# Kernel optimization log

Hardware: AMD Instinct MI355X
Metric: run time of the kernel (lower is better)

The kernel has to match this reference:

```python
import jax, jax.numpy as jnp
import numpy as np

B, S, P, D = 128, 64, 32, 256   # batch, seq_len, pad_size, input_size
E, H, L, A, O = 256, 128, 2, 1, 2  # embed, hidden, n_layers, att_dim, output
INITRANGE = 0.1


def setup_inputs() -> dict:
    key = jax.random.key(0)
    ks = jax.random.split(key, 12)
    u = lambda k, shape: jax.random.uniform(k, shape, jnp.float32, -INITRANGE, INITRANGE)
    return {
        "inputs": jax.random.normal(ks[0], (B, S, P, D), jnp.float32),
        "conv_w": u(ks[1], (D,)),          # Conv1d(1,1,kernel=D) weight (output length is 1)
        "conv_b": u(ks[2], (1,)),
        "embed_w": u(ks[3], (E, D)),       # Linear(D,E,bias=False)
        "gru_Wih": u(ks[4], (L, 2, 3 * H, E)),  # [layer, direction, 3H, in] (E == 2H)
        "gru_Whh": u(ks[5], (L, 2, 3 * H, H)),
        "gru_bih": u(ks[6], (L, 2, 3 * H)),
        "gru_bhh": u(ks[7], (L, 2, 3 * H)),
        "att_w1": u(ks[8], (A, 2 * H)),    # Linear(2H, att_dim, bias=False)
        "lin_w": u(ks[9], (O, 2 * H)),
        "lin_b": u(ks[10], (O,)),
        "batch_size": B,
    }


def _gru_layer(x, Wih, Whh, bih, bhh, reverse):
    # x: [B,S,Din]; torch GRU cell semantics.
    xg = jnp.einsum('bsd,gd->sbg', x, Wih) + bih  # precompute input gates [S,B,3H]
    h0 = jnp.zeros((x.shape[0], Whh.shape[1]), x.dtype)

    def step(h, xg_t):
        gh = h @ Whh.T + bhh
        xr, xz, xn = jnp.split(xg_t, 3, axis=-1)
        hr, hz, hn = jnp.split(gh, 3, axis=-1)
        r = jax.nn.sigmoid(xr + hr)
        z = jax.nn.sigmoid(xz + hz)
        n = jnp.tanh(xn + r * hn)
        h_new = (1.0 - z) * n + z * h
        return h_new, h_new

    _, hs = jax.lax.scan(step, h0, xg, reverse=reverse)  # [S,B,H], time-aligned
    return jnp.swapaxes(hs, 0, 1)  # [B,S,H]


def _forward(inputs, conv_w, conv_b, embed_w, gru_Wih, gru_Whh, gru_bih, gru_bhh,
             att_w1, lin_w, lin_b, batch_size):
    # convolutional_layer: conv output length is 1 -> per-event scalar dot product,
    # then bmm gives a weighted sum of events within each visit.
    s = jnp.einsum('bspk,k->bsp', inputs, conv_w) + conv_b[0]      # [B,S,P]
    conv_all = jnp.einsum('bsp,bspk->bsk', s, inputs)               # [B,S,D]
    # embedding_layer: Linear(D,E) + Hardtanh
    x = jnp.clip(conv_all @ embed_w.T, -1.0, 1.0)                   # [B,S,E]
    # bidirectional multi-layer GRU, h0 = zeros (dropout_p = 0 -> identity)
    for l in range(L):
        f = _gru_layer(x, gru_Wih[l, 0], gru_Whh[l, 0], gru_bih[l, 0], gru_bhh[l, 0], False)
        b = _gru_layer(x, gru_Wih[l, 1], gru_Whh[l, 1], gru_bih[l, 1], gru_bhh[l, 1], True)
        x = jnp.concatenate([f, b], axis=-1)                        # [B,S,2H]
    states = x
    # add_attention: per-step Linear(2H, att_dim) + softmax over att_dim (nn.Softmax on [B,A])
    alpha = jax.nn.softmax(jnp.einsum('bsh,ah->bsa', states, att_w1), axis=-1)
    alpha = jnp.swapaxes(alpha, 1, 2)                               # [B,A,S]
    context = jnp.einsum('bas,bsh->bah', alpha, states).reshape(batch_size, -1)  # [B, A*2H]
    out = jax.nn.softmax(context @ lin_w.T + lin_b, axis=-1)        # [B,O]
    return out, states, context, alpha


def reference(inputs, conv_w, conv_b, embed_w, gru_Wih, gru_Whh, gru_bih, gru_bhh,
              att_w1, lin_w, lin_b, batch_size):
    return _forward(inputs, conv_w, conv_b, embed_w, gru_Wih, gru_Whh, gru_bih,
                    gru_bhh, att_w1, lin_w, lin_b, batch_size)
```

## Files before the change

### kernel.cpp

```cpp
#include <hip/hip_runtime.h>


using u16 = unsigned short;
using u32 = unsigned int;

typedef __bf16    bf16x8 __attribute__((ext_vector_type(8)));
typedef _Float16  f16x8  __attribute__((ext_vector_type(8)));
typedef float     f32x4  __attribute__((ext_vector_type(4)));

__device__ __forceinline__ float bf2f(u16 u) {
  union { u32 i; float f; } v; v.i = ((u32)u) << 16; return v.f;
}
__device__ __forceinline__ u16 f2bf(float f) {
  union { float f; u32 i; } v; v.f = f;
  u32 i = v.i;
  u32 r = (i + 0x7FFFu + ((i >> 16) & 1u)) >> 16;
  return (u16)r;
}
__device__ __forceinline__ float sigm(float x) { return 1.f / (1.f + __expf(-x)); }
__device__ __forceinline__ float tanh_f(float x) { return 1.f - 2.f / (1.f + __expf(2.f * x)); }

__global__ __launch_bounds__(256) void k_conv(
    const float* __restrict__ inp, const float* __restrict__ cw,
    const float* __restrict__ cb, u16* __restrict__ chi, u16* __restrict__ clo,
    const float* __restrict__ embw, const float* __restrict__ Wih,
    u16* __restrict__ embHi, u16* __restrict__ embLo, u16* __restrict__ wihB) {
  __shared__ float tile[32 * 256];
  __shared__ float cwf[256];
  __shared__ float s_p[32];
  const int bs  = blockIdx.x;
  const int tid = threadIdx.x;
  const float* src = inp + (size_t)bs * 8192;
#pragma unroll
  for (int i = 0; i < 8; i++) {
    int idx = i * 1024 + tid * 4;
    *(float4*)&tile[idx] = *(const float4*)&src[idx];
  }
  cwf[tid] = cw[tid];
  if (bs < 1536) {
    const int i = bs * 256 + tid;
    if (i < 65536) {
      float v = embw[i];
      u16 h = f2bf(v);
      embHi[i] = h;
      embLo[i] = f2bf(v - bf2f(h));
    }
    wihB[i] = f2bf(Wih[i]);
  }
  __syncthreads();
  const int wv = tid >> 6, ln = tid & 63;
  const float cbf = cb[0];
  for (int pp = 0; pp < 8; pp++) {
    int p = wv * 8 + pp;
    float part = 0.f;
#pragma unroll
    for (int q = 0; q < 4; q++) {
      int k = ln + q * 64;
      part += tile[p * 256 + k] * cwf[k];
    }
    for (int off = 32; off; off >>= 1) part += __shfl_xor(part, off, 64);
    if (ln == 0) s_p[p] = part + cbf;
  }
  __syncthreads();
  float acc = 0.f;
  const int k = tid;
#pragma unroll
  for (int p = 0; p < 32; p++) acc += s_p[p] * tile[p * 256 + k];
  u16 hi = f2bf(acc);
  float lo = acc - bf2f(hi);
  chi[(size_t)bs * 256 + k] = hi;
  clo[(size_t)bs * 256 + k] = f2bf(lo);
}

template <bool HAS_ALO, bool HAS_WLO, bool HAS_BIAS, bool CLIP, bool OUT_BF16>
__global__ __launch_bounds__(256) void k_gemm(
    const u16* __restrict__ A, const u16* __restrict__ Alo,
    const u16* __restrict__ W, const u16* __restrict__ Wlo,
    const float* __restrict__ bias,
    void* __restrict__ Cout, int M, int N, int K) {
  const int LDT = 56;
  __shared__ u16 As[64 * 56];
  __shared__ u16 La[64 * 56];
  __shared__ u16 Ws[64 * 56];
  __shared__ u16 Lw[64 * 56];
  const int tid = threadIdx.x;
  const int m0 = blockIdx.x * 64, n0 = blockIdx.y * 64;
  const int wv = tid >> 6, ln = tid & 63;
  const int lm = ln & 15, lk = (ln >> 4) * 8;
  const int srow = tid >> 2, sgrp = tid & 3;

  const size_t aRow = (size_t)(m0 + srow) * K + sgrp * 8;
  const size_t wRow = (size_t)(n0 + srow) * K + sgrp * 8;

  f32x4 acc[4];
#pragma unroll
  for (int nt = 0; nt < 4; nt++) acc[nt] = (f32x4){0.f, 0.f, 0.f, 0.f};

  uint4 rA = *(const uint4*)&A[aRow];
  uint4 rW = *(const uint4*)&W[wRow];
  uint4 rLa, rLw;
  if (HAS_ALO) rLa = *(const uint4*)&Alo[aRow];
  if (HAS_WLO) rLw = *(const uint4*)&Wlo[wRow];

  const int nIter = K >> 5;
  for (int it = 0; it < nIter; it++) {
    __syncthreads();
    *(uint4*)&As[srow * LDT + sgrp * 8] = rA;
    *(uint4*)&Ws[srow * LDT + sgrp * 8] = rW;
    if (HAS_ALO) *(uint4*)&La[srow * LDT + sgrp * 8] = rLa;
    if (HAS_WLO) *(uint4*)&Lw[srow * LDT + sgrp * 8] = rLw;
    if (it + 1 < nIter) {
      const int kc = (it + 1) * 32;
      rA = *(const uint4*)&A[aRow + kc];
      rW = *(const uint4*)&W[wRow + kc];
      if (HAS_ALO) rLa = *(const uint4*)&Alo[aRow + kc];
      if (HAS_WLO) rLw = *(const uint4*)&Wlo[wRow + kc];
    }
    __syncthreads();

    bf16x8 af = *(const bf16x8*)&As[(wv * 16 + lm) * LDT + lk];
    bf16x8 bfr[4];
#pragma unroll
    for (int nt = 0; nt < 4; nt++)
      bfr[nt] = *(const bf16x8*)&Ws[(nt * 16 + lm) * LDT + lk];
#pragma unroll
    for (int nt = 0; nt < 4; nt++)
      acc[nt] = __builtin_amdgcn_mfma_f32_16x16x32_bf16(af, bfr[nt], acc[nt], 0, 0, 0);
    if (HAS_ALO) {
      bf16x8 lf = *(const bf16x8*)&La[(wv * 16 + lm) * LDT + lk];
#pragma unroll
      for (int nt = 0; nt < 4; nt++)
        acc[nt] = __builtin_amdgcn_mfma_f32_16x16x32_bf16(lf, bfr[nt], acc[nt], 0, 0, 0);
    }
    if (HAS_WLO) {
#pragma unroll
      for (int nt = 0; nt < 4; nt++) {
        bf16x8 wl = *(const bf16x8*)&Lw[(nt * 16 + lm) * LDT + lk];
        acc[nt] = __builtin_amdgcn_mfma_f32_16x16x32_bf16(af, wl, acc[nt], 0, 0, 0);
      }
    }
  }

  const int rbase = m0 + wv * 16 + (ln >> 4) * 4;
#pragma unroll
  for (int nt = 0; nt < 4; nt++) {
    const int col = n0 + nt * 16 + lm;
    const float bv = HAS_BIAS ? bias[col] : 0.f;
#pragma unroll
    for (int r = 0; r < 4; r++) {
      float v = acc[nt][r] + bv;
      if (CLIP) v = fminf(fmaxf(v, -1.f), 1.f);
      const int row = rbase + r;
      if (OUT_BF16)
        ((u16*)Cout)[(size_t)row * N + col] = f2bf(v);
      else
        ((float*)Cout)[(size_t)row * N + col] = v;
    }
  }
}

__global__ __launch_bounds__(512, 2) void k_gru(
    const u16* __restrict__ xsrc,
    const u16* __restrict__ wihL,
    const float* __restrict__ bihL,
    const float* __restrict__ WhhL,
    const float* __restrict__ bhhL,
    float* __restrict__ xg,
    u16* __restrict__ st_bf,
    float* __restrict__ st_f,
    float* __restrict__ ctx) {
  __shared__ __attribute__((aligned(16))) u16 xt[64 * 264];
  __shared__ __attribute__((aligned(16))) _Float16 hbHi[2][128];
  __shared__ __attribute__((aligned(16))) _Float16 hbLo[2][128];

  const int b   = blockIdx.x >> 1;
  const int dir = blockIdx.x & 1;
  const int tid = threadIdx.x;
  const int w   = tid >> 6, l = tid & 63;
  const int lm  = l & 15;
  const int kw  = (l >> 4) * 8;
  const int d   = w * 16 + lm;

  f16x8 whi[3][4], wlo[3][4];
#pragma unroll
  for (int tt = 0; tt < 3; tt++) {
#pragma unroll
    for (int kt = 0; kt < 4; kt++) {
      const int row = (tt * 8 + w) * 16 + lm;
      const float* p = WhhL + ((size_t)(dir * 384 + row)) * 128 + kt * 32 + kw;
      union { f16x8 v; _Float16 s[8]; } Wh, Wl;
#pragma unroll
      for (int j = 0; j < 8; j++) {
        float v = p[j];
        _Float16 h = (_Float16)v;
        Wh.s[j] = h;
        Wl.s[j] = (_Float16)(v - (float)h);
      }
      whi[tt][kt] = Wh.v;
      wlo[tt][kt] = Wl.v;
    }
  }

  const u16*   wihD = wihL + (size_t)dir * 98304;
  const float* bihD = bihL + dir * 384;
  float*       xgc  = xg + (size_t)(b * 2 + dir) * 24576;
  {
    const u16* xrow = xsrc + (size_t)(b * 64) * 256;
#pragma unroll
    for (int it = 0; it < 4; it++) {
      const int idx = it * 512 + tid;
      const int r = idx >> 5, c8 = (idx & 31) * 8;
      *(uint4*)&xt[r * 264 + c8] = *(const uint4*)&xrow[r * 256 + c8];
    }
    __syncthreads();
#pragma unroll
    for (int tt = 0; tt < 3; tt++) {
      const int nt = tt * 8 + w;
      bf16x8 bfr[8];
#pragma unroll
      for (int kk = 0; kk < 8; kk++)
        bfr[kk] = *(const bf16x8*)&wihD[(size_t)(nt * 16 + lm) * 256 + kk * 32 + kw];
      const float bv = bihD[nt * 16 + lm];
      const int col = nt * 16 + lm;
#pragma unroll
      for (int mt = 0; mt < 4; mt++) {
        f32x4 a4 = (f32x4){0.f, 0.f, 0.f, 0.f};
#pragma unroll
        for (int kk = 0; kk < 8; kk++) {
          bf16x8 af = *(const bf16x8*)&xt[(mt * 16 + lm) * 264 + kk * 32 + kw];
          a4 = __builtin_amdgcn_mfma_f32_16x16x32_bf16(af, bfr[kk], a4, 0, 0, 0);
        }
        const int trow = mt * 16 + (l >> 4) * 4;
#pragma unroll
        for (int r = 0; r < 4; r++)
          xgc[(size_t)(trow + r) * 384 + col] = a4[r] + bv;
      }
    }
  }
  float bhr = 0.f, bhz = 0.f, bhn = 0.f;
  if (l < 16) {
    bhr = bhhL[dir * 384 + d];
    bhz = bhhL[dir * 384 + 128 + d];
    bhn = bhhL[dir * 384 + 256 + d];
  }
  if (tid < 128) { hbHi[0][tid] = (_Float16)0.f; hbLo[0][tid] = (_Float16)0.f; }
  __syncthreads();

  const float* xbase = xgc + d;
  float xr = 0.f, xz = 0.f, xn = 0.f;
  if (l < 16) {
    const int t0 = dir ? 63 : 0;
    xr = xbase[t0 * 384];
    xz = xbase[t0 * 384 + 128];
    xn = xbase[t0 * 384 + 256];
  }
  float hold = 0.f, csum = 0.f;

  int cur = 0;
  for (int ti = 0; ti < 64; ti++) {
    const int t = dir ? (63 - ti) : ti;
    float nxr = 0.f, nxz = 0.f, nxn = 0.f;
    if (l < 16 && ti < 63) {
      const int tn = dir ? (62 - ti) : (ti + 1);
      nxr = xbase[tn * 384];
      nxz = xbase[tn * 384 + 128];
      nxn = xbase[tn * 384 + 256];
    }
    const _Float16* hsrc = (l & 1) ? hbLo[cur] : hbHi[cur];
    f16x8 af[4];
#pragma unroll
    for (int kt = 0; kt < 4; kt++)
      af[kt] = *(const f16x8*)&hsrc[kt * 32 + kw];

    f32x4 aH[3], aL[3];
#pragma unroll
    for (int tt = 0; tt < 3; tt++) {
      aH[tt] = (f32x4){0.f, 0.f, 0.f, 0.f};
      aL[tt] = (f32x4){0.f, 0.f, 0.f, 0.f};
    }
#pragma unroll
    for (int kt = 0; kt < 4; kt++) {
#pragma unroll
      for (int tt = 0; tt < 3; tt++) {
        aH[tt] = __builtin_amdgcn_mfma_f32_16x16x32_f16(af[kt], whi[tt][kt], aH[tt], 0, 0, 0);
        aL[tt] = __builtin_amdgcn_mfma_f32_16x16x32_f16(af[kt], wlo[tt][kt], aL[tt], 0, 0, 0);
      }
    }
    const int nxt = cur ^ 1;
    if (l < 16) {
      const float ghr = aH[0][0] + aH[0][1] + aL[0][0] + aL[0][1];
      const float ghz = aH[1][0] + aH[1][1] + aL[1][0] + aL[1][1];
      const float ghn = aH[2][0] + aH[2][1] + aL[2][0] + aL[2][1];
      const float rg = sigm(xr + bhr + ghr);
      const float zg = sigm(xz + bhz + ghz);
      const float ng = tanh_f(xn + rg * (ghn + bhn));
      const float hn = (1.f - zg) * ng + zg * hold;
      hold = hn;
      csum += hn;
      const _Float16 hh = (_Float16)hn;
      hbHi[nxt][d] = hh;
      hbLo[nxt][d] = (_Float16)(hn - (float)hh);
      const size_t oi = (size_t)(b * 64 + t) * 256 + dir * 128 + d;
      if (st_bf) st_bf[oi] = f2bf(hn);
      if (st_f)  st_f[oi]  = hn;
    }
    asm volatile("s_waitcnt lgkmcnt(0)" ::: "memory");
    __builtin_amdgcn_s_barrier();
    cur = nxt;
    xr = nxr; xz = nxz; xn = nxn;
  }
  if (ctx != nullptr && l < 16)
    ctx[(size_t)b * 256 + dir * 128 + d] = csum;
}

__global__ __launch_bounds__(64) void k_final(
    const float* __restrict__ ctx, const float* __restrict__ lw,
    const float* __restrict__ lb, float* __restrict__ out,
    float* __restrict__ alpha) {
  const int b = blockIdx.x;
  const int l = threadIdx.x;
  float a0 = 0.f, a1 = 0.f;
#pragma unroll
  for (int q = 0; q < 4; q++) {
    const int k = q * 64 + l;
    const float c = ctx[b * 256 + k];
    a0 += c * lw[k];
    a1 += c * lw[256 + k];
  }
  for (int off = 32; off; off >>= 1) {
    a0 += __shfl_xor(a0, off, 64);
    a1 += __shfl_xor(a1, off, 64);
  }
  alpha[b * 64 + l] = 1.0f;
  if (l == 0) {
    a0 += lb[0];
    a1 += lb[1];
    const float m = fmaxf(a0, a1);
    const float e0 = __expf(a0 - m), e1 = __expf(a1 - m);
    const float s = e0 + e1;
    out[2 * b]     = e0 / s;
    out[2 * b + 1] = e1 / s;
  }
}

extern "C" void kernel_launch(void* const* d_in, const int* in_sizes, int n_in,
                              void* d_out, int out_size, void* d_ws, size_t ws_size,
                              hipStream_t stream) {
  const float* inp   = (const float*)d_in[0];
  const float* convw = (const float*)d_in[1];
  const float* convb = (const float*)d_in[2];
  const float* embw  = (const float*)d_in[3];
  const float* Wih   = (const float*)d_in[4];
  const float* Whh   = (const float*)d_in[5];
  const float* bih   = (const float*)d_in[6];
  const float* bhh   = (const float*)d_in[7];
  const float* lw    = (const float*)d_in[9];
  const float* lb    = (const float*)d_in[10];

  char* ws = (char*)d_ws;
  u16*   convHi = (u16*)(ws);
  u16*   convLo = (u16*)(ws + 4194304u);
  u16*   xbuf   = (u16*)(ws + 8388608u);
  u16*   embHi  = (u16*)(ws + 12582912u);
  u16*   embLo  = (u16*)(ws + 12713984u);
  u16*   wihB   = (u16*)(ws + 12845056u);
  float* xgbuf  = (float*)(ws + 13631488u);
  u16*   states0 = convHi;

  float* outp    = (float*)d_out;
  float* statesO = outp + 256;
  float* ctxO    = outp + 2097408;
  float* alphaO  = outp + 2130176;

  k_conv<<<8192, 256, 0, stream>>>(inp, convw, convb, convHi, convLo,
                                   embw, Wih, embHi, embLo, wihB);

  dim3 gE(128, 4);
  k_gemm<true, true, false, true, true><<<gE, 256, 0, stream>>>(
      convHi, convLo, embHi, embLo, nullptr, xbuf, 8192, 256, 256);

  k_gru<<<256, 512, 0, stream>>>(xbuf, wihB, bih, Whh, bhh, xgbuf,
                                 states0, nullptr, nullptr);

  k_gru<<<256, 512, 0, stream>>>(states0, wihB + 196608, bih + 768,
                                 Whh + 98304, bhh + 768, xgbuf,
                                 nullptr, statesO, ctxO);

  k_final<<<128, 64, 0, stream>>>(ctxO, lw, lb, outp, alphaO);
}
```

Before: 528.1 us.

## Fuse embedding GEMM into first GRU layer kernel

Measured after the change: 541.0 us. 1.02x slower.

```diff
diff --git a/kernel.cpp b/kernel.cpp
--- a/kernel.cpp
+++ b/kernel.cpp
@@ -72,95 +72,13 @@
   clo[(size_t)bs * 256 + k] = f2bf(lo);
 }
 
-template <bool HAS_ALO, bool HAS_WLO, bool HAS_BIAS, bool CLIP, bool OUT_BF16>
-__global__ __launch_bounds__(256) void k_gemm(
-    const u16* __restrict__ A, const u16* __restrict__ Alo,
-    const u16* __restrict__ W, const u16* __restrict__ Wlo,
-    const float* __restrict__ bias,
-    void* __restrict__ Cout, int M, int N, int K) {
-  const int LDT = 56;
-  __shared__ u16 As[64 * 56];
-  __shared__ u16 La[64 * 56];
-  __shared__ u16 Ws[64 * 56];
-  __shared__ u16 Lw[64 * 56];
-  const int tid = threadIdx.x;
-  const int m0 = blockIdx.x * 64, n0 = blockIdx.y * 64;
-  const int wv = tid >> 6, ln = tid & 63;
-  const int lm = ln & 15, lk = (ln >> 4) * 8;
-  const int srow = tid >> 2, sgrp = tid & 3;
-
-  const size_t aRow = (size_t)(m0 + srow) * K + sgrp * 8;
-  const size_t wRow = (size_t)(n0 + srow) * K + sgrp * 8;
-
-  f32x4 acc[4];
-#pragma unroll
-  for (int nt = 0; nt < 4; nt++) acc[nt] = (f32x4){0.f, 0.f, 0.f, 0.f};
-
-  uint4 rA = *(const uint4*)&A[aRow];
-  uint4 rW = *(const uint4*)&W[wRow];
-  uint4 rLa, rLw;
-  if (HAS_ALO) rLa = *(const uint4*)&Alo[aRow];
-  if (HAS_WLO) rLw = *(const uint4*)&Wlo[wRow];
-
-  const int nIter = K >> 5;
-  for (int it = 0; it < nIter; it++) {
-    __syncthreads();
-    *(uint4*)&As[srow * LDT + sgrp * 8] = rA;
-    *(uint4*)&Ws[srow * LDT + sgrp * 8] = rW;
-    if (HAS_ALO) *(uint4*)&La[srow * LDT + sgrp * 8] = rLa;
-    if (HAS_WLO) *(uint4*)&Lw[srow * LDT + sgrp * 8] = rLw;
-    if (it + 1 < nIter) {
-      const int kc = (it + 1) * 32;
-      rA = *(const uint4*)&A[aRow + kc];
-      rW = *(const uint4*)&W[wRow + kc];
-      if (HAS_ALO) rLa = *(const uint4*)&Alo[aRow + kc];
-      if (HAS_WLO) rLw = *(const uint4*)&Wlo[wRow + kc];
-    }
-    __syncthreads();
-
-    bf16x8 af = *(const bf16x8*)&As[(wv * 16 + lm) * LDT + lk];
-    bf16x8 bfr[4];
-#pragma unroll
-    for (int nt = 0; nt < 4; nt++)
-      bfr[nt] = *(const bf16x8*)&Ws[(nt * 16 + lm) * LDT + lk];
-#pragma unroll
-    for (int nt = 0; nt < 4; nt++)
-      acc[nt] = __builtin_amdgcn_mfma_f32_16x16x32_bf16(af, bfr[nt], acc[nt], 0, 0, 0);
-    if (HAS_ALO) {
-      bf16x8 lf = *(const bf16x8*)&La[(wv * 16 + lm) * LDT + lk];
-#pragma unroll
-      for (int nt = 0; nt < 4; nt++)
-        acc[nt] = __builtin_amdgcn_mfma_f32_16x16x32_bf16(lf, bfr[nt], acc[nt], 0, 0, 0);
-    }
-    if (HAS_WLO) {
-#pragma unroll
-      for (int nt = 0; nt < 4; nt++) {
-        bf16x8 wl = *(const bf16x8*)&Lw[(nt * 16 + lm) * LDT + lk];
-        acc[nt] = __builtin_amdgcn_mfma_f32_16x16x32_bf16(af, wl, acc[nt], 0, 0, 0);
-      }
-    }
-  }
-
-  const int rbase = m0 + wv * 16 + (ln >> 4) * 4;
-#pragma unroll
-  for (int nt = 0; nt < 4; nt++) {
-    const int col = n0 + nt * 16 + lm;
-    const float bv = HAS_BIAS ? bias[col] : 0.f;
-#pragma unroll
-    for (int r = 0; r < 4; r++) {
-      float v = acc[nt][r] + bv;
-      if (CLIP) v = fminf(fmaxf(v, -1.f), 1.f);
-      const int row = rbase + r;
-      if (OUT_BF16)
-        ((u16*)Cout)[(size_t)row * N + col] = f2bf(v);
-      else
-        ((float*)Cout)[(size_t)row * N + col] = v;
-    }
-  }
-}
-
+template <bool FE>
 __global__ __launch_bounds__(512, 2) void k_gru(
     const u16* __restrict__ xsrc,
+    const u16* __restrict__ convHi,
+    const u16* __restrict__ convLo,
+    const u16* __restrict__ embHi,
+    const u16* __restrict__ embLo,
     const u16* __restrict__ wihL,
     const float* __restrict__ bihL,
     const float* __restrict__ WhhL,
@@ -170,6 +88,8 @@
     float* __restrict__ st_f,
     float* __restrict__ ctx) {
   __shared__ __attribute__((aligned(16))) u16 xt[64 * 264];
+  __shared__ __attribute__((aligned(16))) u16 ah[64 * 264];
+  __shared__ __attribute__((aligned(16))) u16 al[64 * 264];
   __shared__ __attribute__((aligned(16))) _Float16 hbHi[2][128];
   __shared__ __attribute__((aligned(16))) _Float16 hbLo[2][128];
 
@@ -181,6 +101,89 @@
   const int kw  = (l >> 4) * 8;
   const int d   = w * 16 + lm;
 
+  if (FE) {
+    const u16* chiRow = convHi + (size_t)(b * 64) * 256;
+    const u16* cloRow = convLo + (size_t)(b * 64) * 256;
+#pragma unroll
+    for (int it = 0; it < 4; it++) {
+      const int idx = it * 512 + tid;
+      const int r = idx >> 5, c8 = (idx & 31) * 8;
+      *(uint4*)&ah[r * 264 + c8] = *(const uint4*)&chiRow[r * 256 + c8];
+      *(uint4*)&al[r * 264 + c8] = *(const uint4*)&cloRow[r * 256 + c8];
+    }
+    __syncthreads();
+    const int mt = w & 3;
+    const int ntBase = (w >> 2) * 8;
+#pragma unroll
+    for (int np = 0; np < 4; np++) {
+      const int nt0 = ntBase + np * 2, nt1 = nt0 + 1;
+      f32x4 a0 = (f32x4){0.f, 0.f, 0.f, 0.f};
+      f32x4 a1 = (f32x4){0.f, 0.f, 0.f, 0.f};
+#pragma unroll
+      for (int kk = 0; kk < 8; kk++) {
+        bf16x8 ahf = *(const bf16x8*)&ah[(mt * 16 + lm) * 264 + kk * 32 + kw];
+        bf16x8 alf = *(const bf16x8*)&al[(mt * 16 + lm) * 264 + kk * 32 + kw];
+        bf16x8 w0h = *(const bf16x8*)&embHi[(size_t)(nt0 * 16 + lm) * 256 + kk * 32 + kw];
+        bf16x8 w0l = *(const bf16x8*)&embLo[(size_t)(nt0 * 16 + lm) * 256 + kk * 32 + kw];
+        bf16x8 w1h = *(const bf16x8*)&embHi[(size_t)(nt1 * 16 + lm) * 256 + kk * 32 + kw];
+        bf16x8 w1l = *(const bf16x8*)&embLo[(size_t)(nt1 * 16 + lm) * 256 + kk * 32 + kw];
+        a0 = __builtin_amdgcn_mfma_f32_16x16x32_bf16(ahf, w0h, a0, 0, 0, 0);
+        a0 = __builtin_amdgcn_mfma_f32_16x16x32_bf16(alf, w0h, a0, 0, 0, 0);
+        a0 = __builtin_amdgcn_mfma_f32_16x16x32_bf16(ahf, w0l, a0, 0, 0, 0);
+        a1 = __builtin_amdgcn_mfma_f32_16x16x32_bf16(ahf, w1h, a1, 0, 0, 0);
+        a1 = __builtin_amdgcn_mfma_f32_16x16x32_bf16(alf, w1h, a1, 0, 0, 0);
+        a1 = __builtin_amdgcn_mfma_f32_16x16x32_bf16(ahf, w1l, a1, 0, 0, 0);
+      }
+      const int trow = mt * 16 + (l >> 4) * 4;
+#pragma unroll
+      for (int r = 0; r < 4; r++) {
+        float v0 = fminf(fmaxf(a0[r], -1.f), 1.f);
+        float v1 = fminf(fmaxf(a1[r], -1.f), 1.f);
+        xt[(trow + r) * 264 + nt0 * 16 + lm] = f2bf(v0);
+        xt[(trow + r) * 264 + nt1 * 16 + lm] = f2bf(v1);
+      }
+    }
+    __syncthreads();
+  } else {
+    const u16* xrow = xsrc + (size_t)(b * 64) * 256;
+#pragma unroll
+    for (int it = 0; it < 4; it++) {
+      const int idx = it * 512 + tid;
+      const int r = idx >> 5, c8 = (idx & 31) * 8;
+      *(uint4*)&xt[r * 264 + c8] = *(const uint4*)&xrow[r * 256 + c8];
+    }
+    __syncthreads();
+  }
+
+  const u16*   wihD = wihL + (size_t)dir * 98304;
+  const float* bihD = bihL + dir * 384;
+  float*       xgc  = xg + (size_t)(b * 2 + dir) * 24576;
+  {
+#pragma unroll
+    for (int tt = 0; tt < 3; tt++) {
+      const int nt = tt * 8 + w;
+      bf16x8 bfr[8];
+#pragma unroll
+      for (int kk = 0; kk < 8; kk++)
+        bfr[kk] = *(const bf16x8*)&wihD[(size_t)(nt * 16 + lm) * 256 + kk * 32 + kw];
+      const float bv = bihD[nt * 16 + lm];
+      const int col = nt * 16 + lm;
+#pragma unroll
+      for (int mt = 0; mt < 4; mt++) {
+        f32x4 a4 = (f32x4){0.f, 0.f, 0.f, 0.f};
+#pragma unroll
+        for (int kk = 0; kk < 8; kk++) {
+          bf16x8 af = *(const bf16x8*)&xt[(mt * 16 + lm) * 264 + kk * 32 + kw];
+          a4 = __builtin_amdgcn_mfma_f32_16x16x32_bf16(af, bfr[kk], a4, 0, 0, 0);
+        }
+        const int trow = mt * 16 + (l >> 4) * 4;
+#pragma unroll
+        for (int r = 0; r < 4; r++)
+          xgc[(size_t)(trow + r) * 384 + col] = a4[r] + bv;
+      }
+    }
+  }
+
   f16x8 whi[3][4], wlo[3][4];
 #pragma unroll
   for (int tt = 0; tt < 3; tt++) {
@@ -198,43 +201,6 @@
       }
       whi[tt][kt] = Wh.v;
       wlo[tt][kt] = Wl.v;
-    }
-  }
-
-  const u16*   wihD = wihL + (size_t)dir * 98304;
-  const float* bihD = bihL + dir * 384;
-  float*       xgc  = xg + (size_t)(b * 2 + dir) * 24576;
-  {
-    const u16* xrow = xsrc + (size_t)(b * 64) * 256;
-#pragma unroll
-    for (int it = 0; it < 4; it++) {
-      const int idx = it * 512 + tid;
-      const int r = idx >> 5, c8 = (idx & 31) * 8;
-      *(uint4*)&xt[r * 264 + c8] = *(const uint4*)&xrow[r * 256 + c8];
-    }
-    __syncthreads();
-#pragma unroll
-    for (int tt = 0; tt < 3; tt++) {
-      const int nt = tt * 8 + w;
-      bf16x8 bfr[8];
-#pragma unroll
-      for (int kk = 0; kk < 8; kk++)
-        bfr[kk] = *(const bf16x8*)&wihD[(size_t)(nt * 16 + lm) * 256 + kk * 32 + kw];
-      const float bv = bihD[nt * 16 + lm];
-      const int col = nt * 16 + lm;
-#pragma unroll
-      for (int mt = 0; mt < 4; mt++) {
-        f32x4 a4 = (f32x4){0.f, 0.f, 0.f, 0.f};
-#pragma unroll
-        for (int kk = 0; kk < 8; kk++) {
-          bf16x8 af = *(const bf16x8*)&xt[(mt * 16 + lm) * 264 + kk * 32 + kw];
-          a4 = __builtin_amdgcn_mfma_f32_16x16x32_bf16(af, bfr[kk], a4, 0, 0, 0);
-        }
-        const int trow = mt * 16 + (l >> 4) * 4;
-#pragma unroll
-        for (int r = 0; r < 4; r++)
-          xgc[(size_t)(trow + r) * 384 + col] = a4[r] + bv;
-      }
     }
   }
   float bhr = 0.f, bhz = 0.f, bhn = 0.f;
@@ -360,12 +326,11 @@
   char* ws = (char*)d_ws;
   u16*   convHi = (u16*)(ws);
   u16*   convLo = (u16*)(ws + 4194304u);
-  u16*   xbuf   = (u16*)(ws + 8388608u);
+  u16*   states0 = (u16*)(ws + 8388608u);
   u16*   embHi  = (u16*)(ws + 12582912u);
   u16*   embLo  = (u16*)(ws + 12713984u);
   u16*   wihB   = (u16*)(ws + 12845056u);
   float* xgbuf  = (float*)(ws + 13631488u);
-  u16*   states0 = convHi;
 
   float* outp    = (float*)d_out;
   float* statesO = outp + 256;
@@ -375,16 +340,14 @@
   k_conv<<<8192, 256, 0, stream>>>(inp, convw, convb, convHi, convLo,
                                    embw, Wih, embHi, embLo, wihB);
 
-  dim3 gE(128, 4);
-  k_gemm<true, true, false, true, true><<<gE, 256, 0, stream>>>(
-      convHi, convLo, embHi, embLo, nullptr, xbuf, 8192, 256, 256);
-
-  k_gru<<<256, 512, 0, stream>>>(xbuf, wihB, bih, Whh, bhh, xgbuf,
-                                 states0, nullptr, nullptr);
-
-  k_gru<<<256, 512, 0, stream>>>(states0, wihB + 196608, bih + 768,
-                                 Whh + 98304, bhh + 768, xgbuf,
-                                 nullptr, statesO, ctxO);
+  k_gru<true><<<256, 512, 0, stream>>>(
+      nullptr, convHi, convLo, embHi, embLo,
+      wihB, bih, Whh, bhh, xgbuf, states0, nullptr, nullptr);
+
+  k_gru<false><<<256, 512, 0, stream>>>(
+      states0, nullptr, nullptr, nullptr, nullptr,
+      wihB + 196608, bih + 768, Whh + 98304, bhh + 768, xgbuf,
+      nullptr, statesO, ctxO);
 
   k_final<<<128, 64, 0, stream>>>(ctxO, lw, lb, outp, alphaO);
 }
```
